# Optimization experiments

Hardware: AMD Instinct MI355X
Metric: run time of the kernel (lower is better)

Reference implementation:

```python
import jax, jax.numpy as jnp
import numpy as np
from jax import lax

B, S, H = 4, 512, 2048
E, D = 16, 128
GH = E * D  # GRU hidden size = num_experts * router_dim
BAL_STRENGTH = 0.01


def _l2norm(v, eps):
    n = jnp.linalg.norm(v, axis=-1, keepdims=True)
    return v / jnp.maximum(n, eps)


def setup_inputs() -> dict:
    key = jax.random.key(0)
    ks = jax.random.split(key, 6)
    x = jax.random.normal(ks[0], (B, S, H), dtype=jnp.float32)
    hn = jax.random.normal(ks[1], (1, B, GH), dtype=jnp.float32)
    w_ih = jax.random.normal(ks[2], (3 * GH, H), dtype=jnp.float32) * 0.02
    w_hh = jax.random.normal(ks[3], (3 * GH, GH), dtype=jnp.float32) * 0.02
    w_expr = jax.random.normal(ks[4], (H, GH), dtype=jnp.float32) * 0.02
    expert_load_ema = jax.random.uniform(ks[5], (E,), dtype=jnp.float32)
    return {"x": x, "hn": hn, "w_ih": w_ih, "w_hh": w_hh,
            "w_expr": w_expr, "expert_load_ema": expert_load_ema, "top_k": 2}


def _gru(x, h0, w_ih, w_hh):
    # PyTorch GRU (no bias): gates ordered (r, z, n). Precompute input proj once.
    xi = jnp.einsum('bsh,gh->sbg', x, w_ih)  # [S,B,3*GH]
    xr, xz, xn = jnp.split(xi, 3, axis=-1)
    wr, wz, wn = jnp.split(w_hh, 3, axis=0)

    def step(h, xs):
        xr_t, xz_t, xn_t = xs
        r = jax.nn.sigmoid(xr_t + h @ wr.T)
        z = jax.nn.sigmoid(xz_t + h @ wz.T)
        n = jnp.tanh(xn_t + r * (h @ wn.T))
        h = (1.0 - z) * n + z * h
        return h, h

    hT, hs = lax.scan(step, h0, (xr, xz, xn))
    return hs.transpose(1, 0, 2), hT[None]  # [B,S,GH], [1,B,GH]


def reference(x, hn, w_ih, w_hh, w_expr, expert_load_ema, top_k):
    b, s, _ = x.shape
    e = expert_load_ema.shape[0]
    gh = w_hh.shape[1]
    d = gh // e

    routing_logits, hn_out = _gru(x, hn[0], w_ih, w_hh)

    expression_logits = (x @ w_expr).reshape(b, s, e, d)
    rout = routing_logits.reshape(b, s, e, d)
    rout = _l2norm(rout, 1e-12)  # F.normalize(dim=-1)

    # per-token expert gram matrix [B,S,E,E]
    gram = jnp.einsum('bsed,bsfd->bsef', rout, rout)
    diff = gram - jnp.eye(e, dtype=rout.dtype)
    diffn = _l2norm(diff, 1e-12)
    speciality_penalty = jnp.mean(jnp.sum(diffn ** 2, axis=(-2, -1)))

    # cosine sim (rout already unit-norm)
    en = jnp.maximum(jnp.linalg.norm(expression_logits, axis=-1), 1e-8)
    rn = jnp.maximum(jnp.linalg.norm(rout, axis=-1), 1e-8)
    cos = jnp.sum(expression_logits * rout, axis=-1) / (en * rn)
    cosine_similarities = 1.0 - cos  # [B,S,E]

    domain = (cosine_similarities * (1.0 + speciality_penalty)).reshape(b * s, e)
    top_vals, selected_experts = lax.top_k(domain, top_k)
    multiplier = jax.nn.softmax(top_vals.astype(jnp.float32), axis=-1).astype(domain.dtype)

    # ExpressionProjector orthogonal loss
    gw = w_expr.T @ w_expr
    expression_loss = jnp.mean((gw - jnp.eye(gh, dtype=w_expr.dtype)) ** 2)

    # training-mode EMA load-balance adjustment (no_grad in torch)
    ema = lax.stop_gradient(expert_load_ema)
    total = ema.sum()
    scores = jnp.where(total > 0, ema / jnp.maximum(total, 1e-12), jnp.zeros_like(ema))
    adjustment = scores * BAL_STRENGTH * e
    multiplier = multiplier - adjustment[selected_experts]

    return (multiplier, selected_experts, expression_logits, hn_out,
            speciality_penalty, cosine_similarities, expression_loss)
```

## Files before the change

kernel.cpp:

```cpp
#include <hip/hip_runtime.h>
#include <hip/hip_bf16.h>
#include <math.h>

#define BB 4
#define SS 512
#define HH 2048
#define EE 16
#define DD 128
#define GH 2048
#define G3 6144
#define NTOK 2048

#define LSTR 132
#define FPAD 32
#define KS 40

typedef __attribute__((ext_vector_type(8))) short short8;
typedef __attribute__((ext_vector_type(4))) float f32x4;

__global__ __launch_bounds__(256) void gemm_abt(const float* __restrict__ A,
                                                const float* __restrict__ B,
                                                float* __restrict__ C,
                                                int M, int N, int K) {
  __shared__ float As[8][LSTR];
  __shared__ float Bs[8][LSTR];
  const int bm = blockIdx.y * 128, bn = blockIdx.x * 128;
  const int tid = threadIdx.x;
  const int lm = tid >> 1;
  const int kh = (tid & 1) * 4;
  const int tx = tid & 15, ty = tid >> 4;
  float acc[8][8] = {};
  const float* Arow = A + (size_t)(bm + lm) * K + kh;
  const float* Brow = B + (size_t)(bn + lm) * K + kh;
  for (int k0 = 0; k0 < K; k0 += 8) {
    float4 av = *(const float4*)(Arow + k0);
    float4 bv = *(const float4*)(Brow + k0);
    As[kh + 0][lm] = av.x; As[kh + 1][lm] = av.y; As[kh + 2][lm] = av.z; As[kh + 3][lm] = av.w;
    Bs[kh + 0][lm] = bv.x; Bs[kh + 1][lm] = bv.y; Bs[kh + 2][lm] = bv.z; Bs[kh + 3][lm] = bv.w;
    __syncthreads();
#pragma unroll
    for (int kk = 0; kk < 8; ++kk) {
      float a8[8], b8[8];
      *(float4*)(a8)     = *(const float4*)(&As[kk][ty * 8]);
      *(float4*)(a8 + 4) = *(const float4*)(&As[kk][ty * 8 + 4]);
      *(float4*)(b8)     = *(const float4*)(&Bs[kk][tx * 8]);
      *(float4*)(b8 + 4) = *(const float4*)(&Bs[kk][tx * 8 + 4]);
#pragma unroll
      for (int i = 0; i < 8; ++i)
#pragma unroll
        for (int j = 0; j < 8; ++j) acc[i][j] = fmaf(a8[i], b8[j], acc[i][j]);
    }
    __syncthreads();
  }
#pragma unroll
  for (int i = 0; i < 8; ++i) {
    float4 v0 = {acc[i][0], acc[i][1], acc[i][2], acc[i][3]};
    float4 v1 = {acc[i][4], acc[i][5], acc[i][6], acc[i][7]};
    float* crow = C + (size_t)(bm + ty * 8 + i) * N + bn + tx * 8;
    *(float4*)(crow)     = v0;
    *(float4*)(crow + 4) = v1;
  }
}

__global__ __launch_bounds__(256) void gemm_ab(const float* __restrict__ A,
                                               const float* __restrict__ B,
                                               float* __restrict__ C,
                                               int M, int N, int K) {
  __shared__ float As[8][LSTR];
  __shared__ float Bs[8][LSTR];
  const int bm = blockIdx.y * 128, bn = blockIdx.x * 128;
  const int tid = threadIdx.x;
  const int lm = tid >> 1;
  const int kh = (tid & 1) * 4;
  const int bk = tid >> 5;
  const int bn4 = (tid & 31) * 4;
  const int tx = tid & 15, ty = tid >> 4;
  float acc[8][8] = {};
  const float* Arow = A + (size_t)(bm + lm) * K + kh;
  for (int k0 = 0; k0 < K; k0 += 8) {
    float4 av = *(const float4*)(Arow + k0);
    float4 bv = *(const float4*)(B + (size_t)(k0 + bk) * N + bn + bn4);
    As[kh + 0][lm] = av.x; As[kh + 1][lm] = av.y; As[kh + 2][lm] = av.z; As[kh + 3][lm] = av.w;
    *(float4*)(&Bs[bk][bn4]) = bv;
    __syncthreads();
#pragma unroll
    for (int kk = 0; kk < 8; ++kk) {
      float a8[8], b8[8];
      *(float4*)(a8)     = *(const float4*)(&As[kk][ty * 8]);
      *(float4*)(a8 + 4) = *(const float4*)(&As[kk][ty * 8 + 4]);
      *(float4*)(b8)     = *(const float4*)(&Bs[kk][tx * 8]);
      *(float4*)(b8 + 4) = *(const float4*)(&Bs[kk][tx * 8 + 4]);
#pragma unroll
      for (int i = 0; i < 8; ++i)
#pragma unroll
        for (int j = 0; j < 8; ++j) acc[i][j] = fmaf(a8[i], b8[j], acc[i][j]);
    }
    __syncthreads();
  }
#pragma unroll
  for (int i = 0; i < 8; ++i) {
    float4 v0 = {acc[i][0], acc[i][1], acc[i][2], acc[i][3]};
    float4 v1 = {acc[i][4], acc[i][5], acc[i][6], acc[i][7]};
    float* crow = C + (size_t)(bm + ty * 8 + i) * N + bn + tx * 8;
    *(float4*)(crow)     = v0;
    *(float4*)(crow + 4) = v1;
  }
}

__global__ __launch_bounds__(256) void ata_loss(const float* __restrict__ A,
                                                float* __restrict__ el_accum,
                                                int N, int K) {
  __shared__ float As[8][LSTR];
  __shared__ float Bs[8][LSTR];
  __shared__ float red[256];
  const int bi = blockIdx.y * 128, bj = blockIdx.x * 128;
  const int tid = threadIdx.x;
  const int bk = tid >> 5;
  const int bn4 = (tid & 31) * 4;
  const int tx = tid & 15, ty = tid >> 4;
  float acc[8][8] = {};
  for (int k0 = 0; k0 < K; k0 += 8) {
    float4 av = *(const float4*)(A + (size_t)(k0 + bk) * N + bi + bn4);
    float4 bv = *(const float4*)(A + (size_t)(k0 + bk) * N + bj + bn4);
    *(float4*)(&As[bk][bn4]) = av;
    *(float4*)(&Bs[bk][bn4]) = bv;
    __syncthreads();
#pragma unroll
    for (int kk = 0; kk < 8; ++kk) {
      float a8[8], b8[8];
      *(float4*)(a8)     = *(const float4*)(&As[kk][ty * 8]);
      *(float4*)(a8 + 4) = *(const float4*)(&As[kk][ty * 8 + 4]);
      *(float4*)(b8)     = *(const float4*)(&Bs[kk][tx * 8]);
      *(float4*)(b8 + 4) = *(const float4*)(&Bs[kk][tx * 8 + 4]);
#pragma unroll
      for (int i = 0; i < 8; ++i)
#pragma unroll
        for (int j = 0; j < 8; ++j) acc[i][j] = fmaf(a8[i], b8[j], acc[i][j]);
    }
    __syncthreads();
  }
  float local = 0.f;
#pragma unroll
  for (int i = 0; i < 8; ++i) {
#pragma unroll
    for (int j = 0; j < 8; ++j) {
      int gi = bi + ty * 8 + i, gj = bj + tx * 8 + j;
      float d = acc[i][j] - ((gi == gj) ? 1.0f : 0.0f);
      local += d * d;
    }
  }
  red[tid] = local;
  __syncthreads();
  for (int s = 128; s > 0; s >>= 1) {
    if (tid < s) red[tid] += red[tid + s];
    __syncthreads();
  }
  if (tid == 0) atomicAdd(el_accum, red[0]);
}

__device__ inline void bf16_split(float v, unsigned short& hi, unsigned short& lo) {
  unsigned u = __float_as_uint(v);
  unsigned r = u + 0x7FFFu + ((u >> 16) & 1u);
  hi = (unsigned short)(r >> 16);
  float rem = v - __uint_as_float((unsigned)hi << 16);
  lo = (unsigned short)(__float_as_uint(rem) >> 16);
}

__global__ __launch_bounds__(256) void split_mat(const float* __restrict__ A,
                                                 unsigned short* __restrict__ Hh,
                                                 unsigned short* __restrict__ Hl,
                                                 int n) {
  int i = blockIdx.x * 256 + threadIdx.x;
  int stride = gridDim.x * 256;
  for (; i < n; i += stride) {
    unsigned short hi, lo;
    bf16_split(A[i], hi, lo);
    Hh[i] = hi; Hl[i] = lo;
  }
}

__global__ __launch_bounds__(256) void transpose_split(const float* __restrict__ A,
                                                       unsigned short* __restrict__ Th,
                                                       unsigned short* __restrict__ Tl) {
  __shared__ float tile[64][65];
  const int bx = blockIdx.x * 64, by = blockIdx.y * 64;
  const int tx = threadIdx.x & 63, ty = threadIdx.x >> 6;
#pragma unroll
  for (int i = 0; i < 16; ++i) {
    int r = ty + i * 4;
    tile[r][tx] = A[(size_t)(by + r) * GH + bx + tx];
  }
  __syncthreads();
#pragma unroll
  for (int i = 0; i < 16; ++i) {
    int r = ty + i * 4;
    unsigned short hi, lo;
    bf16_split(tile[tx][r], hi, lo);
    Th[(size_t)(bx + r) * HH + by + tx] = hi;
    Tl[(size_t)(bx + r) * HH + by + tx] = lo;
  }
}

__global__ __launch_bounds__(256) void gemm_abt_bf16(
    const unsigned short* __restrict__ Ah, const unsigned short* __restrict__ Al,
    const unsigned short* __restrict__ Bh, const unsigned short* __restrict__ Bl,
    float* __restrict__ C, int M, int N, int K) {
  __shared__ unsigned short Ahs[128 * KS], Als[128 * KS];
  __shared__ unsigned short Bhs[128 * KS], Bls[128 * KS];
  const int tid = threadIdx.x;
  const int wv = tid >> 6, lane = tid & 63;
  const int qr = wv >> 1, qc = wv & 1;
  const int m16 = lane & 15, q = lane >> 4;
  const int bm = blockIdx.y * 128, bn = blockIdx.x * 128;
  const int sr = tid >> 1, sh = (tid & 1) * 16;
  f32x4 zero = {0.f, 0.f, 0.f, 0.f};
  f32x4 acc[4][4];
#pragma unroll
  for (int i = 0; i < 4; ++i)
#pragma unroll
    for (int j = 0; j < 4; ++j) acc[i][j] = zero;

  for (int k0 = 0; k0 < K; k0 += 32) {
    const size_t ga = (size_t)(bm + sr) * K + k0 + sh;
    const size_t gb = (size_t)(bn + sr) * K + k0 + sh;
    short8 a0 = *(const short8*)(Ah + ga);
    short8 a1 = *(const short8*)(Ah + ga + 8);
    short8 l0 = *(const short8*)(Al + ga);
    short8 l1 = *(const short8*)(Al + ga + 8);
    short8 b0 = *(const short8*)(Bh + gb);
    short8 b1 = *(const short8*)(Bh + gb + 8);
    short8 m0 = *(const short8*)(Bl + gb);
    short8 m1 = *(const short8*)(Bl + gb + 8);
    __syncthreads();
    *(short8*)&Ahs[sr * KS + sh]     = a0;
    *(short8*)&Ahs[sr * KS + sh + 8] = a1;
    *(short8*)&Als[sr * KS + sh]     = l0;
    *(short8*)&Als[sr * KS + sh + 8] = l1;
    *(short8*)&Bhs[sr * KS + sh]     = b0;
    *(short8*)&Bhs[sr * KS + sh + 8] = b1;
    *(short8*)&Bls[sr * KS + sh]     = m0;
    *(short8*)&Bls[sr * KS + sh + 8] = m1;
    __syncthreads();
    short8 afh[4], afl[4], bfh[4], bfl[4];
#pragma unroll
    for (int t = 0; t < 4; ++t) {
      const int raddr = (qr * 64 + t * 16 + m16) * KS + q * 8;
      const int caddr = (qc * 64 + t * 16 + m16) * KS + q * 8;
      afh[t] = *(const short8*)&Ahs[raddr];
      afl[t] = *(const short8*)&Als[raddr];
      bfh[t] = *(const short8*)&Bhs[caddr];
      bfl[t] = *(const short8*)&Bls[caddr];
    }
#pragma unroll
    for (int tm = 0; tm < 4; ++tm)
#pragma unroll
      for (int tn = 0; tn < 4; ++tn) {
        acc[tm][tn] = __builtin_amdgcn_mfma_f32_16x16x32_bf16(afh[tm], bfh[tn], acc[tm][tn], 0, 0, 0);
        acc[tm][tn] = __builtin_amdgcn_mfma_f32_16x16x32_bf16(afh[tm], bfl[tn], acc[tm][tn], 0, 0, 0);
        acc[tm][tn] = __builtin_amdgcn_mfma_f32_16x16x32_bf16(afl[tm], bfh[tn], acc[tm][tn], 0, 0, 0);
      }
  }
#pragma unroll
  for (int tm = 0; tm < 4; ++tm)
#pragma unroll
    for (int tn = 0; tn < 4; ++tn)
#pragma unroll
      for (int r = 0; r < 4; ++r)
        C[(size_t)(bm + qr * 64 + tm * 16 + q * 4 + r) * N +
          bn + qc * 64 + tn * 16 + m16] = acc[tm][tn][r];
}

__global__ __launch_bounds__(256) void ata_bf16(
    const unsigned short* __restrict__ Th, const unsigned short* __restrict__ Tl,
    float* __restrict__ el_accum, int N, int K) {
  __shared__ unsigned short Ahs[128 * KS], Als[128 * KS];
  __shared__ unsigned short Bhs[128 * KS], Bls[128 * KS];
  __shared__ float red[256];
  const int tid = threadIdx.x;
  const int wv = tid >> 6, lane = tid & 63;
  const int qr = wv >> 1, qc = wv & 1;
  const int m16 = lane & 15, q = lane >> 4;
  const int bi = blockIdx.y * 128, bj = blockIdx.x * 128;
  const int sr = tid >> 1, sh = (tid & 1) * 16;
  f32x4 zero = {0.f, 0.f, 0.f, 0.f};
  f32x4 acc[4][4];
#pragma unroll
  for (int i = 0; i < 4; ++i)
#pragma unroll
    for (int j = 0; j < 4; ++j) acc[i][j] = zero;

  for (int k0 = 0; k0 < K; k0 += 32) {
    const size_t ga = (size_t)(bi + sr) * K + k0 + sh;
    const size_t gb = (size_t)(bj + sr) * K + k0 + sh;
    short8 a0 = *(const short8*)(Th + ga);
    short8 a1 = *(const short8*)(Th + ga + 8);
    short8 l0 = *(const short8*)(Tl + ga);
    short8 l1 = *(const short8*)(Tl + ga + 8);
    short8 b0 = *(const short8*)(Th + gb);
    short8 b1 = *(const short8*)(Th + gb + 8);
    short8 m0 = *(const short8*)(Tl + gb);
    short8 m1 = *(const short8*)(Tl + gb + 8);
    __syncthreads();
    *(short8*)&Ahs[sr * KS + sh]     = a0;
    *(short8*)&Ahs[sr * KS + sh + 8] = a1;
    *(short8*)&Als[sr * KS + sh]     = l0;
    *(short8*)&Als[sr * KS + sh + 8] = l1;
    *(short8*)&Bhs[sr * KS + sh]     = b0;
    *(short8*)&Bhs[sr * KS + sh + 8] = b1;
    *(short8*)&Bls[sr * KS + sh]     = m0;
    *(short8*)&Bls[sr * KS + sh + 8] = m1;
    __syncthreads();
    short8 afh[4], afl[4], bfh[4], bfl[4];
#pragma unroll
    for (int t = 0; t < 4; ++t) {
      const int raddr = (qr * 64 + t * 16 + m16) * KS + q * 8;
      const int caddr = (qc * 64 + t * 16 + m16) * KS + q * 8;
      afh[t] = *(const short8*)&Ahs[raddr];
      afl[t] = *(const short8*)&Als[raddr];
      bfh[t] = *(const short8*)&Bhs[caddr];
      bfl[t] = *(const short8*)&Bls[caddr];
    }
#pragma unroll
    for (int tm = 0; tm < 4; ++tm)
#pragma unroll
      for (int tn = 0; tn < 4; ++tn) {
        acc[tm][tn] = __builtin_amdgcn_mfma_f32_16x16x32_bf16(afh[tm], bfh[tn], acc[tm][tn], 0, 0, 0);
        acc[tm][tn] = __builtin_amdgcn_mfma_f32_16x16x32_bf16(afh[tm], bfl[tn], acc[tm][tn], 0, 0, 0);
        acc[tm][tn] = __builtin_amdgcn_mfma_f32_16x16x32_bf16(afl[tm], bfh[tn], acc[tm][tn], 0, 0, 0);
      }
  }
  float local = 0.f;
#pragma unroll
  for (int tm = 0; tm < 4; ++tm)
#pragma unroll
    for (int tn = 0; tn < 4; ++tn)
#pragma unroll
      for (int r = 0; r < 4; ++r) {
        int gi = bi + qr * 64 + tm * 16 + q * 4 + r;
        int gj = bj + qc * 64 + tn * 16 + m16;
        float d = acc[tm][tn][r] - ((gi == gj) ? 1.0f : 0.0f);
        local += d * d;
      }
  red[tid] = local;
  __syncthreads();
  for (int s = 128; s > 0; s >>= 1) {
    if (tid < s) red[tid] += red[tid + s];
    __syncthreads();
  }
  if (tid == 0) atomicAdd(el_accum, red[0]);
}

template <int CTRL>
__device__ inline float dpp_add(float v) {
  int t = __builtin_amdgcn_update_dpp(0, __float_as_int(v), CTRL, 0xf, 0xf, false);
  return v + __int_as_float(t);
}
__device__ inline float wred64(float v) {
  v = dpp_add<0x121>(v);
  v = dpp_add<0x122>(v);
  v = dpp_add<0x124>(v);
  v = dpp_add<0x128>(v);
  v += __shfl_xor(v, 16);
  v += __shfl_xor(v, 32);
  return v;
}

__global__ __launch_bounds__(512, 2) void gru_persistent(
    const float* __restrict__ xi,
    const float* __restrict__ w_hh,
    const float* __restrict__ hn,
    float* __restrict__ hsx,
    int* __restrict__ flags) {
  __shared__ __align__(16) float hsm[BB * GH];
  const int tid = threadIdx.x;
  const int wave = tid >> 6, lane = tid & 63;
  const int j = blockIdx.x * 8 + wave;

  float wgr[32], wgz[32], wgn[32];
  {
    const float* pr = w_hh + (size_t)j * GH;
    const float* pz = w_hh + (size_t)(GH + j) * GH;
    const float* pn = w_hh + (size_t)(2 * GH + j) * GH;
#pragma unroll
    for (int c = 0; c < 32; ++c) {
      int k = c * 64 + lane;
      wgr[c] = pr[k]; wgz[c] = pz[k]; wgn[c] = pn[k];
    }
  }
#pragma unroll
  for (int i = 0; i < 4; ++i) {
    int k = tid + i * 512;
    float4 v;
    v.x = hn[0 * GH + k]; v.y = hn[1 * GH + k];
    v.z = hn[2 * GH + k]; v.w = hn[3 * GH + k];
    int slot = k ^ ((k >> 3) & 3);
    *(float4*)(&hsm[slot * 4]) = v;
  }
  __syncthreads();

  const int rdo = (lane ^ ((lane >> 3) & 3)) * 4;
  const int hpo = (j ^ ((j >> 3) & 3)) * 4;
  int wslot[4];
#pragma unroll
  for (int i = 0; i < 4; ++i) {
    int k = tid * 4 + i;
    wslot[i] = (k ^ ((k >> 3) & 3)) * 4;
  }

  for (int s = 0; s < SS; ++s) {
    float xr = 0.f, xz = 0.f, xn_ = 0.f;
    if (lane < BB) {
      const float* xrow = xi + ((size_t)(lane * SS + s)) * G3;
      xr  = xrow[j];
      xz  = xrow[GH + j];
      xn_ = xrow[2 * GH + j];
    }

    float ar[BB] = {}, az[BB] = {}, an[BB] = {};
#pragma unroll
    for (int c = 0; c < 32; ++c) {
      float4 h4 = *(const float4*)(&hsm[c * 256 + rdo]);
      float w_r = wgr[c], w_z = wgz[c], w_n = wgn[c];
      ar[0] = fmaf(w_r, h4.x, ar[0]); az[0] = fmaf(w_z, h4.x, az[0]); an[0] = fmaf(w_n, h4.x, an[0]);
      ar[1] = fmaf(w_r, h4.y, ar[1]); az[1] = fmaf(w_z, h4.y, az[1]); an[1] = fmaf(w_n, h4.y, an[1]);
      ar[2] = fmaf(w_r, h4.z, ar[2]); az[2] = fmaf(w_z, h4.z, az[2]); an[2] = fmaf(w_n, h4.z, an[2]);
      ar[3] = fmaf(w_r, h4.w, ar[3]); az[3] = fmaf(w_z, h4.w, az[3]); an[3] = fmaf(w_n, h4.w, an[3]);
    }
#pragma unroll
    for (int b = 0; b < BB; ++b) { ar[b] = wred64(ar[b]); az[b] = wred64(az[b]); an[b] = wred64(an[b]); }

    if (lane < BB) {
      const int b = lane;
      float r = 1.0f / (1.0f + expf(-(xr + ar[b])));
      float z = 1.0f / (1.0f + expf(-(xz + az[b])));
      float n = tanhf(xn_ + r * an[b]);
      float hp = hsm[hpo + b];
      float hv = (1.0f - z) * n + z * hp;
      __hip_atomic_store(hsx + (((size_t)s * 256 + blockIdx.x) * BB + b) * 8 + (j & 7),
                         hv, __ATOMIC_RELAXED, __HIP_MEMORY_SCOPE_AGENT);
    }

    if (s + 1 < SS) {
      __syncthreads();
      if (tid == 0)
        __hip_atomic_store(&flags[blockIdx.x * FPAD], s + 1,
                           __ATOMIC_RELAXED, __HIP_MEMORY_SCOPE_AGENT);
      const int p = tid >> 1;
      const int c4 = (tid & 1) * 4;
      const int want = s + 1;
      while (__hip_atomic_load(&flags[p * FPAD], __ATOMIC_RELAXED,
                               __HIP_MEMORY_SCOPE_AGENT) < want)
        __builtin_amdgcn_s_sleep(1);
      const float* line = hsx + ((size_t)s * 256 + p) * 32 + c4;
      float4 v0 = *(const float4*)(line + 0 * 8);
      float4 v1 = *(const float4*)(line + 1 * 8);
      float4 v2 = *(const float4*)(line + 2 * 8);
      float4 v3 = *(const float4*)(line + 3 * 8);
      *(float4*)(&hsm[wslot[0]]) = float4{v0.x, v1.x, v2.x, v3.x};
      *(float4*)(&hsm[wslot[1]]) = float4{v0.y, v1.y, v2.y, v3.y};
      *(float4*)(&hsm[wslot[2]]) = float4{v0.z, v1.z, v2.z, v3.z};
      *(float4*)(&hsm[wslot[3]]) = float4{v0.w, v1.w, v2.w, v3.w};
      __syncthreads();
    }
  }
}

__device__ inline float red16(float v) {
#pragma unroll
  for (int o = 8; o; o >>= 1) v += __shfl_xor(v, o);
  return v;
}

__global__ __launch_bounds__(256) void token_kernel(const float* __restrict__ hsx,
                                                    const float* __restrict__ expr,
                                                    float* __restrict__ cos_out,
                                                    float* __restrict__ sp_accum) {
  __shared__ float routn[EE * 132];
  __shared__ float rowc[EE];
  const int t = blockIdx.x;
  const int b = t / SS, s = t % SS;
  const int tid = threadIdx.x;
  const int e = tid >> 4, sub = tid & 15;

  const float* rrow = hsx + ((size_t)s * 256 + e * 16 + sub) * 32 + b * 8;
  float rv[8];
  *(float4*)(rv)     = *(const float4*)(rrow);
  *(float4*)(rv + 4) = *(const float4*)(rrow + 4);
  float ss = 0.f;
#pragma unroll
  for (int i = 0; i < 8; ++i) ss += rv[i] * rv[i];
  ss = red16(ss);
  float inv = 1.0f / fmaxf(sqrtf(ss), 1e-12f);
#pragma unroll
  for (int i = 0; i < 8; ++i) {
    rv[i] *= inv;
    routn[e * 132 + sub * 8 + i] = rv[i];
  }

  const float* erow = expr + (size_t)t * GH + e * DD + sub * 8;
  float en2 = 0.f, dot = 0.f;
#pragma unroll
  for (int i = 0; i < 8; ++i) {
    float ev = erow[i];
    en2 += ev * ev;
    dot += ev * rv[i];
  }
  en2 = red16(en2);
  dot = red16(dot);
  if (sub == 0) {
    float cosv = dot / fmaxf(sqrtf(en2), 1e-8f);
    cos_out[t * EE + e] = 1.0f - cosv;
  }
  __syncthreads();

  const int f = sub;
  float g = 0.f;
#pragma unroll
  for (int d = 0; d < DD; ++d)
    g = fmaf(routn[e * 132 + d], routn[f * 132 + d], g);
  float diff = g - ((e == f) ? 1.0f : 0.0f);
  float rowsum = red16(diff * diff);
  if (f == 0) {
    float nrm = fmaxf(sqrtf(rowsum), 1e-12f);
    rowc[e] = rowsum / (nrm * nrm);
  }
  __syncthreads();
  if (tid == 0) {
    float tok = 0.f;
#pragma unroll
    for (int i = 0; i < EE; ++i) tok += rowc[i];
    atomicAdd(sp_accum, tok);
  }
}

__global__ __launch_bounds__(256) void final_kernel(const float* __restrict__ hsx,
                                                    const float* __restrict__ cos_out,
                                                    const float* __restrict__ ema,
                                                    const float* __restrict__ accum,
                                                    float* __restrict__ out_mult,
                                                    float* __restrict__ out_sel,
                                                    float* __restrict__ out_hn,
                                                    float* __restrict__ out_sp,
                                                    float* __restrict__ out_el) {
  const int gtid = blockIdx.x * 256 + threadIdx.x;
  if (gtid < BB * GH) {
    int b = gtid / GH, k = gtid % GH;
    out_hn[gtid] = hsx[((size_t)(SS - 1) * 256 + (k >> 3)) * 32 + b * 8 + (k & 7)];
  }
  if (gtid < NTOK) {
    float sp = accum[0] / (float)NTOK;
    float scale = 1.0f + sp;
    float dv[EE];
#pragma unroll
    for (int e = 0; e < EE; ++e) dv[e] = cos_out[gtid * EE + e] * scale;
    int i0 = 0; float v0 = dv[0];
#pragma unroll
    for (int e = 1; e < EE; ++e) { if (dv[e] > v0) { v0 = dv[e]; i0 = e; } }
    int i1 = -1; float v1 = -1e30f;
#pragma unroll
    for (int e = 0; e < EE; ++e) { if (e != i0 && dv[e] > v1) { v1 = dv[e]; i1 = e; } }
    float ex = expf(v1 - v0);
    float den = 1.0f + ex;
    float m0 = 1.0f / den, m1 = ex / den;
    float total = 0.f;
#pragma unroll
    for (int e = 0; e < EE; ++e) total += ema[e];
    float a0 = 0.f, a1 = 0.f;
    if (total > 0.f) {
      float invt = 1.0f / fmaxf(total, 1e-12f);
      a0 = ema[i0] * invt * 0.01f * (float)EE;
      a1 = ema[i1] * invt * 0.01f * (float)EE;
    }
    out_mult[gtid * 2 + 0] = m0 - a0;
    out_mult[gtid * 2 + 1] = m1 - a1;
    out_sel[gtid * 2 + 0] = (float)i0;
    out_sel[gtid * 2 + 1] = (float)i1;
  }
  if (gtid == 0) {
    out_sp[0] = accum[0] / (float)NTOK;
    out_el[0] = accum[1] / (float)(GH * GH);
  }
}

extern "C" void kernel_launch(void* const* d_in, const int* in_sizes, int n_in,
                              void* d_out, int out_size, void* d_ws, size_t ws_size,
                              hipStream_t stream) {
  const float* x      = (const float*)d_in[0];
  const float* hn     = (const float*)d_in[1];
  const float* w_ih   = (const float*)d_in[2];
  const float* w_hh   = (const float*)d_in[3];
  const float* w_expr = (const float*)d_in[4];
  const float* ema    = (const float*)d_in[5];
  float* out = (float*)d_out;

  float* out_mult = out;
  float* out_sel  = out + 4096;
  float* out_expr = out + 8192;
  float* out_hn   = out + 4202496;
  float* out_sp   = out + 4210688;
  float* out_cos  = out + 4210689;
  float* out_el   = out + 4243457;

  float* ws = (float*)d_ws;
  float* xi    = ws;
  float* hsx   = ws + 12582912;
  float* accum = ws + 16777216;
  int*   flags = (int*)(ws + 16777220);
  unsigned short* xh  = (unsigned short*)(ws + 16785920);
  unsigned short* xl  = (unsigned short*)(ws + 18883072);
  unsigned short* wth = (unsigned short*)(ws + 20980224);
  unsigned short* wtl = (unsigned short*)(ws + 23077376);
  const size_t need_bytes = (size_t)25174528 * 4;
  const bool bf16path = ws_size >= need_bytes;

  hipMemsetAsync(accum, 0, (4 + 256 * FPAD) * sizeof(float), stream);

  gemm_abt<<<dim3(G3 / 128, NTOK / 128), 256, 0, stream>>>(x, w_ih, xi, NTOK, G3, HH);

  if (bf16path) {
    split_mat<<<4096, 256, 0, stream>>>(x, xh, xl, NTOK * HH);
    transpose_split<<<dim3(GH / 64, HH / 64), 256, 0, stream>>>(w_expr, wth, wtl);
    gemm_abt_bf16<<<dim3(GH / 128, NTOK / 128), 256, 0, stream>>>(
        xh, xl, wth, wtl, out_expr, NTOK, GH, HH);
    ata_bf16<<<dim3(GH / 128, GH / 128), 256, 0, stream>>>(wth, wtl, accum + 1, GH, HH);
  } else {
    gemm_ab<<<dim3(GH / 128, NTOK / 128), 256, 0, stream>>>(x, w_expr, out_expr, NTOK, GH, HH);
    ata_loss<<<dim3(GH / 128, GH / 128), 256, 0, stream>>>(w_expr, accum + 1, GH, HH);
  }

  {
    void* args[] = {(void*)&xi, (void*)&w_hh, (void*)&hn, (void*)&hsx, (void*)&flags};
    hipLaunchCooperativeKernel((void*)gru_persistent, dim3(256), dim3(512),
                               args, 0, stream);
  }

  token_kernel<<<NTOK, 256, 0, stream>>>(hsx, out_expr, out_cos, accum);

  final_kernel<<<(BB * GH + 255) / 256, 256, 0, stream>>>(hsx, out_cos, ema, accum,
                                                          out_mult, out_sel, out_hn,
                                                          out_sp, out_el);
}
```

Baseline: 3.898 ms.

## Replace per-block flag barrier with sentinel-valued data polling in GRU kernel

The per-step inter-block sync in the persistent GRU kernel no longer has each block publish a flag that consumers poll. Consumers now spin directly on the hidden-state values, which are pre-filled with a 0xFFFFFFFF NaN sentinel by a memset before launch. This drops one __syncthreads and the flag store/load round trip from each timestep's critical path. In exchange it adds a 16 MB memset per call and relies on relaxed per-element stores becoming visible without a fence, plus on a computed h never having the sentinel bit pattern.

```diff
diff --git a/kernel.cpp b/kernel.cpp
--- a/kernel.cpp
+++ b/kernel.cpp
@@ -369,8 +369,7 @@
     const float* __restrict__ xi,
     const float* __restrict__ w_hh,
     const float* __restrict__ hn,
-    float* __restrict__ hsx,
-    int* __restrict__ flags) {
+    float* __restrict__ hsx) {
   __shared__ __align__(16) float hsm[BB * GH];
   const int tid = threadIdx.x;
   const int wave = tid >> 6, lane = tid & 63;
@@ -406,6 +405,8 @@
     int k = tid * 4 + i;
     wslot[i] = (k ^ ((k >> 3) & 3)) * 4;
   }
+  const int p = tid >> 1;
+  const int c4 = (tid & 1) * 4;
 
   for (int s = 0; s < SS; ++s) {
     float xr = 0.f, xz = 0.f, xn_ = 0.f;
@@ -441,25 +442,26 @@
     }
 
     if (s + 1 < SS) {
-      __syncthreads();
-      if (tid == 0)
-        __hip_atomic_store(&flags[blockIdx.x * FPAD], s + 1,
-                           __ATOMIC_RELAXED, __HIP_MEMORY_SCOPE_AGENT);
-      const int p = tid >> 1;
-      const int c4 = (tid & 1) * 4;
-      const int want = s + 1;
-      while (__hip_atomic_load(&flags[p * FPAD], __ATOMIC_RELAXED,
-                               __HIP_MEMORY_SCOPE_AGENT) < want)
-        __builtin_amdgcn_s_sleep(1);
-      const float* line = hsx + ((size_t)s * 256 + p) * 32 + c4;
-      float4 v0 = *(const float4*)(line + 0 * 8);
-      float4 v1 = *(const float4*)(line + 1 * 8);
-      float4 v2 = *(const float4*)(line + 2 * 8);
-      float4 v3 = *(const float4*)(line + 3 * 8);
-      *(float4*)(&hsm[wslot[0]]) = float4{v0.x, v1.x, v2.x, v3.x};
-      *(float4*)(&hsm[wslot[1]]) = float4{v0.y, v1.y, v2.y, v3.y};
-      *(float4*)(&hsm[wslot[2]]) = float4{v0.z, v1.z, v2.z, v3.z};
-      *(float4*)(&hsm[wslot[3]]) = float4{v0.w, v1.w, v2.w, v3.w};
+      const unsigned* lp =
+          (const unsigned*)(hsx + ((size_t)s * 256 + p) * 32 + c4);
+      float v[16];
+      unsigned pend = 0xFFFFu;
+      do {
+#pragma unroll
+        for (int i = 0; i < 16; ++i) {
+          if (pend & (1u << i)) {
+            unsigned uu = __hip_atomic_load(lp + (i >> 2) * 8 + (i & 3),
+                                            __ATOMIC_RELAXED,
+                                            __HIP_MEMORY_SCOPE_AGENT);
+            if (uu != 0xFFFFFFFFu) { v[i] = __uint_as_float(uu); pend &= ~(1u << i); }
+          }
+        }
+        if (pend) __builtin_amdgcn_s_sleep(1);
+      } while (pend);
+      *(float4*)(&hsm[wslot[0]]) = float4{v[0], v[4], v[8],  v[12]};
+      *(float4*)(&hsm[wslot[1]]) = float4{v[1], v[5], v[9],  v[13]};
+      *(float4*)(&hsm[wslot[2]]) = float4{v[2], v[6], v[10], v[14]};
+      *(float4*)(&hsm[wslot[3]]) = float4{v[3], v[7], v[11], v[15]};
       __syncthreads();
     }
   }
@@ -605,7 +607,6 @@
   float* xi    = ws;
   float* hsx   = ws + 12582912;
   float* accum = ws + 16777216;
-  int*   flags = (int*)(ws + 16777220);
   unsigned short* xh  = (unsigned short*)(ws + 16785920);
   unsigned short* xl  = (unsigned short*)(ws + 18883072);
   unsigned short* wth = (unsigned short*)(ws + 20980224);
@@ -613,7 +614,8 @@
   const size_t need_bytes = (size_t)25174528 * 4;
   const bool bf16path = ws_size >= need_bytes;
 
-  hipMemsetAsync(accum, 0, (4 + 256 * FPAD) * sizeof(float), stream);
+  hipMemsetAsync(accum, 0, 4 * sizeof(float), stream);
+  hipMemsetAsync(hsx, 0xFF, (size_t)4194304 * sizeof(float), stream);
 
   gemm_abt<<<dim3(G3 / 128, NTOK / 128), 256, 0, stream>>>(x, w_ih, xi, NTOK, G3, HH);
 
@@ -629,7 +631,7 @@
   }
 
   {
-    void* args[] = {(void*)&xi, (void*)&w_hh, (void*)&hn, (void*)&hsx, (void*)&flags};
+    void* args[] = {(void*)&xi, (void*)&w_hh, (void*)&hn, (void*)&hsx};
     hipLaunchCooperativeKernel((void*)gru_persistent, dim3(256), dim3(512),
                                args, 0, stream);
   }
```

After: 6.506 ms. +66.9%, slower.

## Split GRU recurrent dot products across K halves and reduce via shared memory

Applied to the files above, without the earlier changes.

Each wave now handles two hidden units over half of the K dimension instead of one unit over all of K, and the two K-halves are combined through a small shared-memory partial buffer. The cross-lane reduction drops the two xor shuffles in favour of DPP row shifts and row broadcasts that leave the full sum in lane 63. This is meant to shorten the per-step serial reduction and raise the FMA work per shared-memory h load. The cost is an extra __syncthreads per timestep and more accumulator registers.

```diff
diff --git a/kernel.cpp b/kernel.cpp
--- a/kernel.cpp
+++ b/kernel.cpp
@@ -355,13 +355,13 @@
   int t = __builtin_amdgcn_update_dpp(0, __float_as_int(v), CTRL, 0xf, 0xf, false);
   return v + __int_as_float(t);
 }
-__device__ inline float wred64(float v) {
-  v = dpp_add<0x121>(v);
-  v = dpp_add<0x122>(v);
-  v = dpp_add<0x124>(v);
-  v = dpp_add<0x128>(v);
-  v += __shfl_xor(v, 16);
-  v += __shfl_xor(v, 32);
+__device__ inline float wred_l63(float v) {
+  v = dpp_add<0x111>(v);
+  v = dpp_add<0x112>(v);
+  v = dpp_add<0x114>(v);
+  v = dpp_add<0x118>(v);
+  v = dpp_add<0x142>(v);
+  v = dpp_add<0x143>(v);
   return v;
 }
 
@@ -372,19 +372,24 @@
     float* __restrict__ hsx,
     int* __restrict__ flags) {
   __shared__ __align__(16) float hsm[BB * GH];
+  __shared__ __align__(16) float part[8][28];
   const int tid = threadIdx.x;
   const int wave = tid >> 6, lane = tid & 63;
-  const int j = blockIdx.x * 8 + wave;
-
-  float wgr[32], wgz[32], wgn[32];
-  {
-    const float* pr = w_hh + (size_t)j * GH;
-    const float* pz = w_hh + (size_t)(GH + j) * GH;
-    const float* pn = w_hh + (size_t)(2 * GH + j) * GH;
-#pragma unroll
-    for (int c = 0; c < 32; ++c) {
-      int k = c * 64 + lane;
-      wgr[c] = pr[k]; wgz[c] = pz[k]; wgn[c] = pn[k];
+  const int kh = wave >> 2;
+  const int cp = wave & 3;
+  const int j0 = blockIdx.x * 8 + cp * 2;
+
+  float wg[2][3][16];
+#pragma unroll
+  for (int cc = 0; cc < 2; ++cc) {
+    const float* pr = w_hh + (size_t)(j0 + cc) * GH + kh * 1024;
+    const float* pz = w_hh + (size_t)(GH + j0 + cc) * GH + kh * 1024;
+    const float* pn = w_hh + (size_t)(2 * GH + j0 + cc) * GH + kh * 1024;
+#pragma unroll
+    for (int c = 0; c < 16; ++c) {
+      wg[cc][0][c] = pr[c * 64 + lane];
+      wg[cc][1][c] = pz[c * 64 + lane];
+      wg[cc][2][c] = pn[c * 64 + lane];
     }
   }
 #pragma unroll
@@ -399,44 +404,70 @@
   __syncthreads();
 
   const int rdo = (lane ^ ((lane >> 3) & 3)) * 4;
-  const int hpo = (j ^ ((j >> 3) & 3)) * 4;
   int wslot[4];
 #pragma unroll
   for (int i = 0; i < 4; ++i) {
     int k = tid * 4 + i;
     wslot[i] = (k ^ ((k >> 3) & 3)) * 4;
   }
+  const int p = tid >> 1;
+  const int c4 = (tid & 1) * 4;
+  const bool gw = (wave < 4);
+  const int gcc = (lane >> 2) & 1, gb = lane & 3;
+  const int gj = blockIdx.x * 8 + wave * 2 + gcc;
+  const int ghpo = (gj ^ ((gj >> 3) & 3)) * 4;
 
   for (int s = 0; s < SS; ++s) {
     float xr = 0.f, xz = 0.f, xn_ = 0.f;
-    if (lane < BB) {
-      const float* xrow = xi + ((size_t)(lane * SS + s)) * G3;
-      xr  = xrow[j];
-      xz  = xrow[GH + j];
-      xn_ = xrow[2 * GH + j];
-    }
-
-    float ar[BB] = {}, az[BB] = {}, an[BB] = {};
-#pragma unroll
-    for (int c = 0; c < 32; ++c) {
-      float4 h4 = *(const float4*)(&hsm[c * 256 + rdo]);
-      float w_r = wgr[c], w_z = wgz[c], w_n = wgn[c];
-      ar[0] = fmaf(w_r, h4.x, ar[0]); az[0] = fmaf(w_z, h4.x, az[0]); an[0] = fmaf(w_n, h4.x, an[0]);
-      ar[1] = fmaf(w_r, h4.y, ar[1]); az[1] = fmaf(w_z, h4.y, az[1]); an[1] = fmaf(w_n, h4.y, an[1]);
-      ar[2] = fmaf(w_r, h4.z, ar[2]); az[2] = fmaf(w_z, h4.z, az[2]); an[2] = fmaf(w_n, h4.z, an[2]);
-      ar[3] = fmaf(w_r, h4.w, ar[3]); az[3] = fmaf(w_z, h4.w, az[3]); an[3] = fmaf(w_n, h4.w, an[3]);
-    }
-#pragma unroll
-    for (int b = 0; b < BB; ++b) { ar[b] = wred64(ar[b]); az[b] = wred64(az[b]); an[b] = wred64(an[b]); }
-
-    if (lane < BB) {
-      const int b = lane;
-      float r = 1.0f / (1.0f + expf(-(xr + ar[b])));
-      float z = 1.0f / (1.0f + expf(-(xz + az[b])));
-      float n = tanhf(xn_ + r * an[b]);
-      float hp = hsm[hpo + b];
+    if (gw && lane < 8) {
+      const float* xrow = xi + ((size_t)(gb * SS + s)) * G3;
+      xr  = xrow[gj];
+      xz  = xrow[GH + gj];
+      xn_ = xrow[2 * GH + gj];
+    }
+
+    float ac[2][3][4] = {};
+#pragma unroll
+    for (int c = 0; c < 16; ++c) {
+      float4 h4 = *(const float4*)(&hsm[(kh * 16 + c) * 256 + rdo]);
+#pragma unroll
+      for (int cc = 0; cc < 2; ++cc)
+#pragma unroll
+        for (int g = 0; g < 3; ++g) {
+          float w = wg[cc][g][c];
+          ac[cc][g][0] = fmaf(w, h4.x, ac[cc][g][0]);
+          ac[cc][g][1] = fmaf(w, h4.y, ac[cc][g][1]);
+          ac[cc][g][2] = fmaf(w, h4.z, ac[cc][g][2]);
+          ac[cc][g][3] = fmaf(w, h4.w, ac[cc][g][3]);
+        }
+    }
+#pragma unroll
+    for (int cc = 0; cc < 2; ++cc)
+#pragma unroll
+      for (int g = 0; g < 3; ++g)
+#pragma unroll
+        for (int b = 0; b < 4; ++b) ac[cc][g][b] = wred_l63(ac[cc][g][b]);
+    if (lane == 63) {
+      *(float4*)(&part[wave][0])  = float4{ac[0][0][0], ac[0][0][1], ac[0][0][2], ac[0][0][3]};
+      *(float4*)(&part[wave][4])  = float4{ac[0][1][0], ac[0][1][1], ac[0][1][2], ac[0][1][3]};
+      *(float4*)(&part[wave][8])  = float4{ac[0][2][0], ac[0][2][1], ac[0][2][2], ac[0][2][3]};
+      *(float4*)(&part[wave][12]) = float4{ac[1][0][0], ac[1][0][1], ac[1][0][2], ac[1][0][3]};
+      *(float4*)(&part[wave][16]) = float4{ac[1][1][0], ac[1][1][1], ac[1][1][2], ac[1][1][3]};
+      *(float4*)(&part[wave][20]) = float4{ac[1][2][0], ac[1][2][1], ac[1][2][2], ac[1][2][3]};
+    }
+    __syncthreads();
+
+    if (gw && lane < 8) {
+      const int qb = gcc * 12 + gb;
+      float rs = part[wave][qb]     + part[wave + 4][qb];
+      float zs = part[wave][qb + 4] + part[wave + 4][qb + 4];
+      float ns = part[wave][qb + 8] + part[wave + 4][qb + 8];
+      float r = 1.0f / (1.0f + expf(-(xr + rs)));
+      float z = 1.0f / (1.0f + expf(-(xz + zs)));
+      float n = tanhf(xn_ + r * ns);
+      float hp = hsm[ghpo + gb];
       float hv = (1.0f - z) * n + z * hp;
-      __hip_atomic_store(hsx + (((size_t)s * 256 + blockIdx.x) * BB + b) * 8 + (j & 7),
+      __hip_atomic_store(hsx + ((size_t)s * 256 + blockIdx.x) * 32 + gb * 8 + (gj & 7),
                          hv, __ATOMIC_RELAXED, __HIP_MEMORY_SCOPE_AGENT);
     }
 
@@ -445,8 +476,6 @@
       if (tid == 0)
         __hip_atomic_store(&flags[blockIdx.x * FPAD], s + 1,
                            __ATOMIC_RELAXED, __HIP_MEMORY_SCOPE_AGENT);
-      const int p = tid >> 1;
-      const int c4 = (tid & 1) * 4;
       const int want = s + 1;
       while (__hip_atomic_load(&flags[p * FPAD], __ATOMIC_RELAXED,
                                __HIP_MEMORY_SCOPE_AGENT) < want)
```

New measurement: 4.268 ms. +9.5%, slower.

## Warp-specialize persistent GRU with fetch waves and double-buffered hidden state

Applied to the files above, without the earlier changes.

The persistent GRU kernel gets two extra waves per block that poll the other blocks' flags and gather the new hidden state into the other half of a double-buffered shared array. Compute waves stop using __syncthreads and wait instead on an LDS ready counter; a per-block arrive counter publishes the global flag once all eight waves have finished a step. The lane-63 DPP row reduction replaces the xor shuffles, and one lane now handles all four batch gate updates. The aim is to cut block-wide barrier cost and let compute of the next step overlap the gather. The cost is more spinning threads, a larger block, double the LDS, and subtle memory-ordering requirements.

```diff
diff --git a/kernel.cpp b/kernel.cpp
--- a/kernel.cpp
+++ b/kernel.cpp
@@ -355,112 +355,156 @@
   int t = __builtin_amdgcn_update_dpp(0, __float_as_int(v), CTRL, 0xf, 0xf, false);
   return v + __int_as_float(t);
 }
-__device__ inline float wred64(float v) {
-  v = dpp_add<0x121>(v);
-  v = dpp_add<0x122>(v);
-  v = dpp_add<0x124>(v);
-  v = dpp_add<0x128>(v);
-  v += __shfl_xor(v, 16);
-  v += __shfl_xor(v, 32);
+__device__ inline float wred_l63(float v) {
+  v = dpp_add<0x111>(v);
+  v = dpp_add<0x112>(v);
+  v = dpp_add<0x114>(v);
+  v = dpp_add<0x118>(v);
+  v = dpp_add<0x142>(v);
+  v = dpp_add<0x143>(v);
   return v;
 }
 
-__global__ __launch_bounds__(512, 2) void gru_persistent(
+__global__ __launch_bounds__(640) void gru_persistent(
     const float* __restrict__ xi,
     const float* __restrict__ w_hh,
     const float* __restrict__ hn,
     float* __restrict__ hsx,
     int* __restrict__ flags) {
-  __shared__ __align__(16) float hsm[BB * GH];
+  __shared__ __align__(16) float hsm[2][BB * GH];
+  __shared__ int arrive_cnt;
+  __shared__ int ready_cnt;
   const int tid = threadIdx.x;
   const int wave = tid >> 6, lane = tid & 63;
-  const int j = blockIdx.x * 8 + wave;
-
-  float wgr[32], wgz[32], wgn[32];
-  {
-    const float* pr = w_hh + (size_t)j * GH;
-    const float* pz = w_hh + (size_t)(GH + j) * GH;
-    const float* pn = w_hh + (size_t)(2 * GH + j) * GH;
-#pragma unroll
-    for (int c = 0; c < 32; ++c) {
-      int k = c * 64 + lane;
-      wgr[c] = pr[k]; wgz[c] = pz[k]; wgn[c] = pn[k];
-    }
-  }
-#pragma unroll
-  for (int i = 0; i < 4; ++i) {
-    int k = tid + i * 512;
-    float4 v;
-    v.x = hn[0 * GH + k]; v.y = hn[1 * GH + k];
-    v.z = hn[2 * GH + k]; v.w = hn[3 * GH + k];
-    int slot = k ^ ((k >> 3) & 3);
-    *(float4*)(&hsm[slot * 4]) = v;
+
+  if (tid == 0) { arrive_cnt = 0; ready_cnt = 0; }
+  if (tid < 512) {
+#pragma unroll
+    for (int i = 0; i < 4; ++i) {
+      int k = tid + i * 512;
+      float4 v;
+      v.x = hn[0 * GH + k]; v.y = hn[1 * GH + k];
+      v.z = hn[2 * GH + k]; v.w = hn[3 * GH + k];
+      int slot = k ^ ((k >> 3) & 3);
+      *(float4*)(&hsm[0][slot * 4]) = v;
+    }
   }
   __syncthreads();
 
-  const int rdo = (lane ^ ((lane >> 3) & 3)) * 4;
-  const int hpo = (j ^ ((j >> 3) & 3)) * 4;
-  int wslot[4];
-#pragma unroll
-  for (int i = 0; i < 4; ++i) {
-    int k = tid * 4 + i;
-    wslot[i] = (k ^ ((k >> 3) & 3)) * 4;
-  }
-
-  for (int s = 0; s < SS; ++s) {
-    float xr = 0.f, xz = 0.f, xn_ = 0.f;
-    if (lane < BB) {
-      const float* xrow = xi + ((size_t)(lane * SS + s)) * G3;
-      xr  = xrow[j];
-      xz  = xrow[GH + j];
-      xn_ = xrow[2 * GH + j];
-    }
-
-    float ar[BB] = {}, az[BB] = {}, an[BB] = {};
-#pragma unroll
-    for (int c = 0; c < 32; ++c) {
-      float4 h4 = *(const float4*)(&hsm[c * 256 + rdo]);
-      float w_r = wgr[c], w_z = wgz[c], w_n = wgn[c];
-      ar[0] = fmaf(w_r, h4.x, ar[0]); az[0] = fmaf(w_z, h4.x, az[0]); an[0] = fmaf(w_n, h4.x, an[0]);
-      ar[1] = fmaf(w_r, h4.y, ar[1]); az[1] = fmaf(w_z, h4.y, az[1]); an[1] = fmaf(w_n, h4.y, an[1]);
-      ar[2] = fmaf(w_r, h4.z, ar[2]); az[2] = fmaf(w_z, h4.z, az[2]); an[2] = fmaf(w_n, h4.z, an[2]);
-      ar[3] = fmaf(w_r, h4.w, ar[3]); az[3] = fmaf(w_z, h4.w, az[3]); an[3] = fmaf(w_n, h4.w, an[3]);
-    }
-#pragma unroll
-    for (int b = 0; b < BB; ++b) { ar[b] = wred64(ar[b]); az[b] = wred64(az[b]); an[b] = wred64(an[b]); }
-
-    if (lane < BB) {
-      const int b = lane;
-      float r = 1.0f / (1.0f + expf(-(xr + ar[b])));
-      float z = 1.0f / (1.0f + expf(-(xz + az[b])));
-      float n = tanhf(xn_ + r * an[b]);
-      float hp = hsm[hpo + b];
-      float hv = (1.0f - z) * n + z * hp;
-      __hip_atomic_store(hsx + (((size_t)s * 256 + blockIdx.x) * BB + b) * 8 + (j & 7),
-                         hv, __ATOMIC_RELAXED, __HIP_MEMORY_SCOPE_AGENT);
-    }
-
-    if (s + 1 < SS) {
-      __syncthreads();
-      if (tid == 0)
-        __hip_atomic_store(&flags[blockIdx.x * FPAD], s + 1,
-                           __ATOMIC_RELAXED, __HIP_MEMORY_SCOPE_AGENT);
-      const int p = tid >> 1;
-      const int c4 = (tid & 1) * 4;
-      const int want = s + 1;
-      while (__hip_atomic_load(&flags[p * FPAD], __ATOMIC_RELAXED,
-                               __HIP_MEMORY_SCOPE_AGENT) < want)
-        __builtin_amdgcn_s_sleep(1);
-      const float* line = hsx + ((size_t)s * 256 + p) * 32 + c4;
-      float4 v0 = *(const float4*)(line + 0 * 8);
-      float4 v1 = *(const float4*)(line + 1 * 8);
-      float4 v2 = *(const float4*)(line + 2 * 8);
-      float4 v3 = *(const float4*)(line + 3 * 8);
-      *(float4*)(&hsm[wslot[0]]) = float4{v0.x, v1.x, v2.x, v3.x};
-      *(float4*)(&hsm[wslot[1]]) = float4{v0.y, v1.y, v2.y, v3.y};
-      *(float4*)(&hsm[wslot[2]]) = float4{v0.z, v1.z, v2.z, v3.z};
-      *(float4*)(&hsm[wslot[3]]) = float4{v0.w, v1.w, v2.w, v3.w};
-      __syncthreads();
+  if (wave < 8) {
+    const int j = blockIdx.x * 8 + wave;
+    float wgr[32], wgz[32], wgn[32];
+    {
+      const float* pr = w_hh + (size_t)j * GH;
+      const float* pz = w_hh + (size_t)(GH + j) * GH;
+      const float* pn = w_hh + (size_t)(2 * GH + j) * GH;
+#pragma unroll
+      for (int c = 0; c < 32; ++c) {
+        int k = c * 64 + lane;
+        wgr[c] = pr[k]; wgz[c] = pz[k]; wgn[c] = pn[k];
+      }
+    }
+    const int rdo = (lane ^ ((lane >> 3) & 3)) * 4;
+    const int hpo = (j ^ ((j >> 3) & 3)) * 4;
+
+    for (int s = 0; s < SS; ++s) {
+      float xr[BB], xz[BB], xn_[BB];
+      if (lane == 63) {
+#pragma unroll
+        for (int b = 0; b < BB; ++b) {
+          const float* xrow = xi + ((size_t)(b * SS + s)) * G3;
+          xr[b]  = xrow[j];
+          xz[b]  = xrow[GH + j];
+          xn_[b] = xrow[2 * GH + j];
+        }
+      }
+      if (s > 0) {
+        const int want = 128 * s;
+        while (__hip_atomic_load(&ready_cnt, __ATOMIC_ACQUIRE,
+                                 __HIP_MEMORY_SCOPE_WORKGROUP) < want)
+          __builtin_amdgcn_s_sleep(1);
+      }
+      const float* cur = hsm[s & 1];
+
+      float ar[BB] = {}, az[BB] = {}, an[BB] = {};
+#pragma unroll
+      for (int c = 0; c < 32; ++c) {
+        float4 h4 = *(const float4*)(&cur[c * 256 + rdo]);
+        float w_r = wgr[c], w_z = wgz[c], w_n = wgn[c];
+        ar[0] = fmaf(w_r, h4.x, ar[0]); az[0] = fmaf(w_z, h4.x, az[0]); an[0] = fmaf(w_n, h4.x, an[0]);
+        ar[1] = fmaf(w_r, h4.y, ar[1]); az[1] = fmaf(w_z, h4.y, az[1]); an[1] = fmaf(w_n, h4.y, an[1]);
+        ar[2] = fmaf(w_r, h4.z, ar[2]); az[2] = fmaf(w_z, h4.z, az[2]); an[2] = fmaf(w_n, h4.z, an[2]);
+        ar[3] = fmaf(w_r, h4.w, ar[3]); az[3] = fmaf(w_z, h4.w, az[3]); an[3] = fmaf(w_n, h4.w, an[3]);
+      }
+#pragma unroll
+      for (int b = 0; b < BB; ++b) {
+        ar[b] = wred_l63(ar[b]); az[b] = wred_l63(az[b]); an[b] = wred_l63(an[b]);
+      }
+
+      if (lane == 63) {
+        float4 hp4 = *(const float4*)(&cur[hpo]);
+        float hpv[BB] = {hp4.x, hp4.y, hp4.z, hp4.w};
+#pragma unroll
+        for (int b = 0; b < BB; ++b) {
+          float r = 1.0f / (1.0f + expf(-(xr[b] + ar[b])));
+          float z = 1.0f / (1.0f + expf(-(xz[b] + az[b])));
+          float n = tanhf(xn_[b] + r * an[b]);
+          float hv = (1.0f - z) * n + z * hpv[b];
+          __hip_atomic_store(hsx + ((size_t)s * 256 + blockIdx.x) * 32 + b * 8 + (j & 7),
+                             hv, __ATOMIC_RELAXED, __HIP_MEMORY_SCOPE_AGENT);
+        }
+      }
+      if (s + 1 < SS) {
+        asm volatile("s_waitcnt vmcnt(0)" ::: "memory");
+        if (lane == 63) {
+          int old = __hip_atomic_fetch_add(&arrive_cnt, 1, __ATOMIC_ACQ_REL,
+                                           __HIP_MEMORY_SCOPE_WORKGROUP);
+          if (old == 8 * (s + 1) - 1)
+            __hip_atomic_store(&flags[blockIdx.x * FPAD], s + 1,
+                               __ATOMIC_RELAXED, __HIP_MEMORY_SCOPE_AGENT);
+        }
+      }
+    }
+  } else {
+    const int f = tid - 512;
+    int cp[4], cc4[4], ws0[4], ws1[4], ws2[4], ws3[4];
+#pragma unroll
+    for (int i = 0; i < 4; ++i) {
+      int c = f + i * 128;
+      cp[i]  = c >> 1;
+      cc4[i] = (c & 1) * 4;
+      int k0 = c * 4;
+      ws0[i] = ((k0 + 0) ^ (((k0 + 0) >> 3) & 3)) * 4;
+      ws1[i] = ((k0 + 1) ^ (((k0 + 1) >> 3) & 3)) * 4;
+      ws2[i] = ((k0 + 2) ^ (((k0 + 2) >> 3) & 3)) * 4;
+      ws3[i] = ((k0 + 3) ^ (((k0 + 3) >> 3) & 3)) * 4;
+    }
+    for (int r = 0; r + 1 < SS; ++r) {
+      float* nb = hsm[(r + 1) & 1];
+      const int want = r + 1;
+      unsigned done = 0;
+      while (done != 0xFu) {
+#pragma unroll
+        for (int i = 0; i < 4; ++i) {
+          if (!(done & (1u << i)) &&
+              __hip_atomic_load(&flags[cp[i] * FPAD], __ATOMIC_RELAXED,
+                                __HIP_MEMORY_SCOPE_AGENT) >= want) {
+            const float* line = hsx + ((size_t)r * 256 + cp[i]) * 32 + cc4[i];
+            float4 v0 = *(const float4*)(line + 0);
+            float4 v1 = *(const float4*)(line + 8);
+            float4 v2 = *(const float4*)(line + 16);
+            float4 v3 = *(const float4*)(line + 24);
+            *(float4*)(&nb[ws0[i]]) = float4{v0.x, v1.x, v2.x, v3.x};
+            *(float4*)(&nb[ws1[i]]) = float4{v0.y, v1.y, v2.y, v3.y};
+            *(float4*)(&nb[ws2[i]]) = float4{v0.z, v1.z, v2.z, v3.z};
+            *(float4*)(&nb[ws3[i]]) = float4{v0.w, v1.w, v2.w, v3.w};
+            done |= 1u << i;
+          }
+        }
+        if (done != 0xFu) __builtin_amdgcn_s_sleep(1);
+      }
+      __hip_atomic_fetch_add(&ready_cnt, 1, __ATOMIC_RELEASE,
+                             __HIP_MEMORY_SCOPE_WORKGROUP);
     }
   }
 }
@@ -630,7 +674,7 @@
 
   {
     void* args[] = {(void*)&xi, (void*)&w_hh, (void*)&hn, (void*)&hsx, (void*)&flags};
-    hipLaunchCooperativeKernel((void*)gru_persistent, dim3(256), dim3(512),
+    hipLaunchCooperativeKernel((void*)gru_persistent, dim3(256), dim3(640),
                                args, 0, stream);
   }
 
```

Result: slower. 3.989 ms (+2.3%).
